# Kernel tuning notes

Measured on AMD Instinct MI355X. Metric: run time of the kernel, lower is better.

The kernel has to match this reference:

```python
import jax, jax.numpy as jnp
import numpy as np

N_NODES = 100000
N_EDGES = 3200000
IN_CH = 35
NUM_FAM = 26
EMBED = 8
NEW_IN = 6 + EMBED + (IN_CH - 6 - NUM_FAM)  # 17
HID = 64
LN_EPS = 1e-5


def setup_inputs() -> dict:
    key = jax.random.key(0)
    ks = jax.random.split(key, 16)
    x = jax.random.normal(ks[0], (N_NODES, IN_CH), dtype=jnp.float32)
    edge_index = jax.random.randint(ks[1], (2, N_EDGES), 0, N_NODES, dtype=jnp.int64)
    s = 0.05
    p = {
        'W_embed': jax.random.normal(ks[2], (NUM_FAM, EMBED), jnp.float32) * s,
        'b_embed': jnp.zeros((EMBED,), jnp.float32),
        'ln_g': jnp.ones((EMBED,), jnp.float32),
        'ln_b': jnp.zeros((EMBED,), jnp.float32),
        'Wl1': jax.random.normal(ks[3], (NEW_IN, HID), jnp.float32) * s,
        'bl1': jnp.zeros((HID,), jnp.float32),
        'Wr1': jax.random.normal(ks[4], (NEW_IN, HID), jnp.float32) * s,
        'Wl2': jax.random.normal(ks[5], (HID, HID), jnp.float32) * s,
        'bl2': jnp.zeros((HID,), jnp.float32),
        'Wr2': jax.random.normal(ks[6], (HID, HID), jnp.float32) * s,
        'Wl3': jax.random.normal(ks[7], (HID, HID), jnp.float32) * s,
        'bl3': jnp.zeros((HID,), jnp.float32),
        'Wr3': jax.random.normal(ks[8], (HID, HID), jnp.float32) * s,
        'Wfc': jax.random.normal(ks[9], (HID, 1), jnp.float32) * s,
        'bfc': jnp.zeros((1,), jnp.float32),
    }
    return {'x': x, 'edge_index': edge_index, **p}


def _sage(h, src, dst, Wl, bl, Wr, n):
    # PyG SAGEConv (mean aggr): lin_l(mean_{j in N(i)} h_j) + lin_r(h_i)
    msum = jax.ops.segment_sum(h[src], dst, num_segments=n)
    cnt = jax.ops.segment_sum(jnp.ones((src.shape[0],), h.dtype), dst, num_segments=n)
    mean = msum / jnp.maximum(cnt, 1.0)[:, None]
    return mean @ Wl + bl + h @ Wr


def reference(x, edge_index, W_embed, b_embed, ln_g, ln_b,
              Wl1, bl1, Wr1, Wl2, bl2, Wr2, Wl3, bl3, Wr3, Wfc, bfc):
    n = x.shape[0]
    src, dst = edge_index[0], edge_index[1]
    node_type = x[:, :6]
    onehot = x[:, 6:6 + NUM_FAM]
    other = x[:, 6 + NUM_FAM:]
    emb = onehot @ W_embed + b_embed
    mu = jnp.mean(emb, axis=-1, keepdims=True)
    var = jnp.var(emb, axis=-1, keepdims=True)
    emb = (emb - mu) * jax.lax.rsqrt(var + LN_EPS) * ln_g + ln_b
    h0 = jnp.concatenate([node_type, emb, other], axis=1)  # [N, 17]
    h1 = jax.nn.relu(_sage(h0, src, dst, Wl1, bl1, Wr1, n))
    h2 = jax.nn.relu(_sage(h1, src, dst, Wl2, bl2, Wr2, n) + h1)
    h3 = jax.nn.relu(_sage(h2, src, dst, Wl3, bl3, Wr3, n) + h2)
    return (h3 @ Wfc + bfc).squeeze(-1)
```

## Files before the change

kernel.cpp:

```cpp
#include <hip/hip_runtime.h>

#define NN 100000
#define NE 3200000
#define NBK 391
#define BCAP2 9216
#define EPB 4096
#define NPB 782

typedef _Float16 half8 __attribute__((ext_vector_type(8)));
typedef float    f32x4 __attribute__((ext_vector_type(4)));

__global__ __launch_bounds__(256) void k_h0(const float* __restrict__ x,
    const float* __restrict__ We, const float* __restrict__ be,
    const float* __restrict__ lg, const float* __restrict__ lb,
    _Float16* __restrict__ h0p)
{
  __shared__ float xs[256 * 35];
  int tid = threadIdx.x;
  int base_node = blockIdx.x * 256;
  int nvalid = NN - base_node; if (nvalid > 256) nvalid = 256;
  int total = nvalid * 35;
  const float* srcp = x + (size_t)base_node * 35;
  for (int j = tid; j < total; j += 256) xs[j] = srcp[j];
  __syncthreads();
  int i = base_node + tid;
  if (i >= NN) return;
  const float* xr = xs + tid * 35;
  float e[8];
  #pragma unroll
  for (int j = 0; j < 8; ++j) e[j] = be[j];
  #pragma unroll
  for (int k = 0; k < 26; ++k) {
    float o = xr[6 + k];
    #pragma unroll
    for (int j = 0; j < 8; ++j) e[j] = fmaf(o, We[k * 8 + j], e[j]);
  }
  float mu = 0.f;
  #pragma unroll
  for (int j = 0; j < 8; ++j) mu += e[j];
  mu *= 0.125f;
  float var = 0.f;
  #pragma unroll
  for (int j = 0; j < 8; ++j) { float d = e[j] - mu; var = fmaf(d, d, var); }
  var *= 0.125f;
  float rs = rsqrtf(var + 1e-5f);

  _Float16 row[32];
  #pragma unroll
  for (int j = 0; j < 6; ++j) row[j] = (_Float16)xr[j];
  #pragma unroll
  for (int j = 0; j < 8; ++j) row[6 + j] = (_Float16)((e[j] - mu) * rs * lg[j] + lb[j]);
  #pragma unroll
  for (int j = 0; j < 3; ++j) row[14 + j] = (_Float16)xr[32 + j];
  #pragma unroll
  for (int j = 17; j < 32; ++j) row[j] = (_Float16)0.f;
  half8* dst = (half8*)(h0p + (size_t)i * 32);
  #pragma unroll
  for (int q = 0; q < 4; ++q) dst[q] = *(half8*)(row + q * 8);
}

__global__ __launch_bounds__(256) void k_partA(const int* __restrict__ ei,
    int* __restrict__ gcur, int* __restrict__ ebuf)
{
  __shared__ int hist[NBK];
  __shared__ int lofs[NBK];
  __shared__ int gb[NBK];
  __shared__ int cur[NBK];
  __shared__ int sd[256];
  __shared__ int stage[EPB];
  __shared__ unsigned short sbkt[EPB];
  int tid = threadIdx.x;
  int base = blockIdx.x * EPB;
  int n = NE - base; if (n > EPB) n = EPB;
  for (int b = tid; b < NBK; b += 256) hist[b] = 0;
  __syncthreads();
  int s[16], d[16];
  #pragma unroll
  for (int k = 0; k < 16; ++k) {
    int idx = tid + k * 256;
    if (idx < n) {
      s[k] = ei[base + idx];
      d[k] = ei[NE + base + idx];
      atomicAdd(&hist[d[k] >> 8], 1);
    } else { s[k] = -1; d[k] = 0; }
  }
  __syncthreads();
  int b0 = 2 * tid, b1 = 2 * tid + 1;
  int c0 = (b0 < NBK) ? hist[b0] : 0;
  int c1 = (b1 < NBK) ? hist[b1] : 0;
  int ls = c0 + c1;
  sd[tid] = ls; __syncthreads();
  for (int off = 1; off < 256; off <<= 1) {
    int t = (tid >= off) ? sd[tid - off] : 0;
    __syncthreads(); sd[tid] += t; __syncthreads();
  }
  int excl = sd[tid] - ls;
  if (b0 < NBK) { lofs[b0] = excl;      cur[b0] = excl;      if (c0) gb[b0] = b0 * BCAP2 + atomicAdd(&gcur[b0], c0); }
  if (b1 < NBK) { lofs[b1] = excl + c0; cur[b1] = excl + c0; if (c1) gb[b1] = b1 * BCAP2 + atomicAdd(&gcur[b1], c1); }
  __syncthreads();
  #pragma unroll
  for (int k = 0; k < 16; ++k) {
    if (s[k] >= 0) {
      int b = d[k] >> 8;
      int p = atomicAdd(&cur[b], 1);
      stage[p] = (s[k] << 8) | (d[k] & 255);
      sbkt[p] = (unsigned short)b;
    }
  }
  __syncthreads();
  for (int p = tid; p < n; p += 256) {
    int b = sbkt[p];
    int pos = gb[b] + (p - lofs[b]);
    if (pos < (b + 1) * BCAP2) ebuf[pos] = stage[p];
  }
}

__global__ __launch_bounds__(512) void k_partB(const int* __restrict__ gcur,
    const int* __restrict__ ebuf, int2* __restrict__ rowinfo, int* __restrict__ srcs)
{
  __shared__ int lcnt[256];
  __shared__ int sd[256];
  int b = blockIdx.x, tid = threadIdx.x;
  int n = gcur[b]; if (n > BCAP2) n = BCAP2;
  const int* eb = ebuf + (size_t)b * BCAP2;
  if (tid < 256) lcnt[tid] = 0;
  __syncthreads();
  for (int e = tid; e < n; e += 512) atomicAdd(&lcnt[eb[e] & 255], 1);
  __syncthreads();
  int v = 0;
  if (tid < 256) { v = lcnt[tid]; sd[tid] = v; }
  __syncthreads();
  for (int off = 1; off < 256; off <<= 1) {
    int t = (tid < 256 && tid >= off) ? sd[tid - off] : 0;
    __syncthreads();
    if (tid < 256) sd[tid] += t;
    __syncthreads();
  }
  if (tid < 256) {
    int excl = sd[tid] - v;
    int node = b * 256 + tid;
    if (node < NN) rowinfo[node] = make_int2(b * BCAP2 + excl, v);
    lcnt[tid] = excl;
  }
  __syncthreads();
  for (int e = tid; e < n; e += 512) {
    int w = eb[e];
    int p = atomicAdd(&lcnt[w & 255], 1);
    srcs[(size_t)b * BCAP2 + p] = w >> 8;
  }
}

template <int W>
__global__ __launch_bounds__(256) void k_agg(const _Float16* __restrict__ hin,
    const int2* __restrict__ rowinfo, const int* __restrict__ srcs,
    _Float16* __restrict__ meanout)
{
  constexpr int GL = W / 8;
  constexpr int NPW = 64 / GL;
  int wave = (blockIdx.x * 256 + threadIdx.x) >> 6;
  int lane = threadIdx.x & 63;
  if (wave * NPW >= NN) return;
  int g = lane / GL;
  int f = lane % GL;
  int node = wave * NPW + g;
  bool valid = node < NN;
  int2 ri = valid ? rowinfo[node] : make_int2(0, 0);
  int rs = ri.x, m = ri.y;
  const int* __restrict__ sp = srcs + rs;

  float acc[8];
  #pragma unroll
  for (int q = 0; q < 8; ++q) acc[q] = 0.f;

  #pragma unroll 4
  for (int e = 0; e < m; ++e) {
    half8 v = *(const half8*)(hin + (size_t)sp[e] * W + f * 8);
    #pragma unroll
    for (int q = 0; q < 8; ++q) acc[q] += (float)v[q];
  }

  if (valid) {
    float r = 1.f / fmaxf((float)m, 1.f);
    _Float16 o[8];
    #pragma unroll
    for (int q = 0; q < 8; ++q) o[q] = (_Float16)(acc[q] * r);
    *(half8*)(meanout + (size_t)node * W + f * 8) = *(half8*)o;
  }
}

template <int W, int KW, bool RES, bool FINAL>
__global__ __launch_bounds__(256) void k_mlp(const _Float16* __restrict__ mean,
    const _Float16* __restrict__ h,
    const float* __restrict__ Wl, const float* __restrict__ bl,
    const float* __restrict__ Wr,
    const float* __restrict__ Wfc, const float* __restrict__ bfc,
    void* __restrict__ outp)
{
  __shared__ _Float16 lwl[64 * W];
  __shared__ _Float16 lwr[64 * W];
  int tid = threadIdx.x;
  for (int idx = tid; idx < 64 * W; idx += 256) {
    int nn = idx / W, kk = idx % W;
    lwl[idx] = (kk < KW) ? (_Float16)Wl[kk * 64 + nn] : (_Float16)0.f;
    lwr[idx] = (kk < KW) ? (_Float16)Wr[kk * 64 + nn] : (_Float16)0.f;
  }
  __syncthreads();
  constexpr int NKB = W / 32;
  int wv = tid >> 6, lane = tid & 63;
  int c = lane & 15, kg = lane >> 4;

  half8 bwl[4][NKB], bwr[4][NKB];
  #pragma unroll
  for (int nt = 0; nt < 4; ++nt)
    #pragma unroll
    for (int kb = 0; kb < NKB; ++kb) {
      bwl[nt][kb] = *(const half8*)&lwl[(nt * 16 + c) * W + kb * 32 + kg * 8];
      bwr[nt][kb] = *(const half8*)&lwr[(nt * 16 + c) * W + kb * 32 + kg * 8];
    }

  int wavebase = blockIdx.x * 256 + wv * 64;
  #pragma unroll
  for (int ti = 0; ti < 4; ++ti) {
    int tbase = wavebase + ti * 16;
    if (tbase >= NN) break;
    half8 am[NKB], ah[NKB];
    #pragma unroll
    for (int kb = 0; kb < NKB; ++kb) {
      am[kb] = *(const half8*)(mean + (size_t)(tbase + c) * W + kb * 32 + kg * 8);
      ah[kb] = *(const half8*)(h    + (size_t)(tbase + c) * W + kb * 32 + kg * 8);
    }
    f32x4 acc[4] = {f32x4{0,0,0,0}, f32x4{0,0,0,0}, f32x4{0,0,0,0}, f32x4{0,0,0,0}};
    #pragma unroll
    for (int nt = 0; nt < 4; ++nt)
      #pragma unroll
      for (int kb = 0; kb < NKB; ++kb) {
        acc[nt] = __builtin_amdgcn_mfma_f32_16x16x32_f16(am[kb], bwl[nt][kb], acc[nt], 0, 0, 0);
        acc[nt] = __builtin_amdgcn_mfma_f32_16x16x32_f16(ah[kb], bwr[nt][kb], acc[nt], 0, 0, 0);
      }
    if (!FINAL) {
      _Float16* hout = (_Float16*)outp;
      #pragma unroll
      for (int nt = 0; nt < 4; ++nt) {
        float bia = bl[nt * 16 + c];
        #pragma unroll
        for (int r = 0; r < 4; ++r) {
          int node = tbase + kg * 4 + r;
          float v = acc[nt][r] + bia;
          if (RES) v += (float)h[(size_t)node * 64 + nt * 16 + c];
          hout[(size_t)node * 64 + nt * 16 + c] = (_Float16)fmaxf(v, 0.f);
        }
      }
    } else {
      #pragma unroll
      for (int r = 0; r < 4; ++r) {
        float p = 0.f;
        #pragma unroll
        for (int nt = 0; nt < 4; ++nt) {
          float v = acc[nt][r] + bl[nt * 16 + c];
          if (RES) v += (float)h[(size_t)(tbase + kg * 4 + r) * 64 + nt * 16 + c];
          v = fmaxf(v, 0.f);
          p = fmaf(v, Wfc[nt * 16 + c], p);
        }
        p += __shfl_xor(p, 1); p += __shfl_xor(p, 2);
        p += __shfl_xor(p, 4); p += __shfl_xor(p, 8);
        if (c == 0) ((float*)outp)[tbase + kg * 4 + r] = p + bfc[0];
      }
    }
  }
}

extern "C" void kernel_launch(void* const* d_in, const int* in_sizes, int n_in,
                              void* d_out, int out_size, void* d_ws, size_t ws_size,
                              hipStream_t stream)
{
  const float* x   = (const float*)d_in[0];
  const int*   ei  = (const int*)d_in[1];
  const float* We  = (const float*)d_in[2];
  const float* be  = (const float*)d_in[3];
  const float* lg  = (const float*)d_in[4];
  const float* lb  = (const float*)d_in[5];
  const float* Wl1 = (const float*)d_in[6];
  const float* bl1 = (const float*)d_in[7];
  const float* Wr1 = (const float*)d_in[8];
  const float* Wl2 = (const float*)d_in[9];
  const float* bl2 = (const float*)d_in[10];
  const float* Wr2 = (const float*)d_in[11];
  const float* Wl3 = (const float*)d_in[12];
  const float* bl3 = (const float*)d_in[13];
  const float* Wr3 = (const float*)d_in[14];
  const float* Wfc = (const float*)d_in[15];
  const float* bfc = (const float*)d_in[16];
  (void)in_sizes; (void)n_in; (void)out_size; (void)ws_size;

  size_t off = 0;
  auto carve = [&](size_t bytes) -> void* {
    void* p = (char*)d_ws + off;
    off += (bytes + 255) & ~(size_t)255;
    return p;
  };
  _Float16* h0p    = (_Float16*)carve((size_t)NN * 32 * 2);
  _Float16* mean1  = (_Float16*)carve((size_t)NN * 32 * 2);
  char*     uni    = (char*)carve((size_t)NBK * BCAP2 * 4);
  int*      ebuf   = (int*)uni;
  _Float16* h1     = (_Float16*)uni;
  _Float16* mean23 = (_Float16*)carve((size_t)NN * 64 * 2);
  _Float16* h2     = (_Float16*)carve((size_t)NN * 64 * 2);
  int*      srcs   = (int*)carve((size_t)NBK * BCAP2 * 4);
  int2*     rowinfo= (int2*)carve((size_t)NN * 8);
  int*      gcur   = (int*)carve((size_t)NBK * 4);

  const int nblk_node  = (NN + 255) / 256;
  const int nblk_agg64 = ((NN + 7) / 8 + 3) / 4;
  const int nblk_agg32 = ((NN + 15) / 16 + 3) / 4;

  hipMemsetAsync(gcur, 0, (size_t)NBK * 4, stream);
  k_h0<<<nblk_node, 256, 0, stream>>>(x, We, be, lg, lb, h0p);
  k_partA<<<NPB, 256, 0, stream>>>(ei, gcur, ebuf);
  k_partB<<<NBK, 512, 0, stream>>>(gcur, ebuf, rowinfo, srcs);

  k_agg<32><<<nblk_agg32, 256, 0, stream>>>(h0p, rowinfo, srcs, mean1);
  k_mlp<32, 17, false, false><<<nblk_node, 256, 0, stream>>>(mean1, h0p, Wl1, bl1, Wr1, nullptr, nullptr, h1);
  k_agg<64><<<nblk_agg64, 256, 0, stream>>>(h1, rowinfo, srcs, mean23);
  k_mlp<64, 64, true, false><<<nblk_node, 256, 0, stream>>>(mean23, h1, Wl2, bl2, Wr2, nullptr, nullptr, h2);
  k_agg<64><<<nblk_agg64, 256, 0, stream>>>(h2, rowinfo, srcs, mean23);
  k_mlp<64, 64, true, true><<<nblk_node, 256, 0, stream>>>(mean23, h2, Wl3, bl3, Wr3, Wfc, bfc, d_out);
}
```

Before: 371.6 us.

## Sort nodes by degree within buckets and batch gather loads in aggregation

During CSR construction each bucket counting-sorts its nodes by in-degree into a permutation array. The aggregation kernels walk nodes through that permutation, so nodes sharing a wave have similar edge counts and lanes diverge less. The edge loop now loads eight neighbour indices and eight feature vectors before accumulating, giving more memory-level parallelism, and it uses shift-based addressing. In exchange it adds a serial prefix scan per block, an extra indirection per node, and output writes that are scattered rather than coalesced.

```diff
diff --git a/kernel.cpp b/kernel.cpp
--- a/kernel.cpp
+++ b/kernel.cpp
@@ -6,6 +6,7 @@
 #define BCAP2 9216
 #define EPB 4096
 #define NPB 782
+#define NSLOT (NBK * 256)
 
 typedef _Float16 half8 __attribute__((ext_vector_type(8)));
 typedef float    f32x4 __attribute__((ext_vector_type(4)));
@@ -116,18 +117,23 @@
 }
 
 __global__ __launch_bounds__(512) void k_partB(const int* __restrict__ gcur,
-    const int* __restrict__ ebuf, int2* __restrict__ rowinfo, int* __restrict__ srcs)
+    const int* __restrict__ ebuf, int2* __restrict__ rowinfo, int* __restrict__ srcs,
+    int* __restrict__ perm)
 {
   __shared__ int lcnt[256];
   __shared__ int sd[256];
+  __shared__ int dhist[128];
+  __shared__ int dcur[128];
   int b = blockIdx.x, tid = threadIdx.x;
   int n = gcur[b]; if (n > BCAP2) n = BCAP2;
   const int* eb = ebuf + (size_t)b * BCAP2;
   if (tid < 256) lcnt[tid] = 0;
+  if (tid >= 256 && tid < 384) dhist[tid - 256] = 0;
+  if (tid < 256) perm[b * 256 + tid] = -1;
   __syncthreads();
   for (int e = tid; e < n; e += 512) atomicAdd(&lcnt[eb[e] & 255], 1);
   __syncthreads();
-  int v = 0;
+  int v = 0, node = b * 256 + tid, dcl = 0;
   if (tid < 256) { v = lcnt[tid]; sd[tid] = v; }
   __syncthreads();
   for (int off = 1; off < 256; off <<= 1) {
@@ -138,11 +144,23 @@
   }
   if (tid < 256) {
     int excl = sd[tid] - v;
-    int node = b * 256 + tid;
-    if (node < NN) rowinfo[node] = make_int2(b * BCAP2 + excl, v);
+    if (node < NN) {
+      rowinfo[node] = make_int2(b * BCAP2 + excl, v);
+      dcl = v < 127 ? v : 127;
+      atomicAdd(&dhist[dcl], 1);
+    }
     lcnt[tid] = excl;
   }
   __syncthreads();
+  if (tid == 0) {
+    int run = 0;
+    for (int d = 0; d < 128; ++d) { int c = dhist[d]; dcur[d] = run; run += c; }
+  }
+  __syncthreads();
+  if (tid < 256 && node < NN) {
+    int p = atomicAdd(&dcur[dcl], 1);
+    perm[b * 256 + p] = node;
+  }
   for (int e = tid; e < n; e += 512) {
     int w = eb[e];
     int p = atomicAdd(&lcnt[w & 255], 1);
@@ -153,17 +171,18 @@
 template <int W>
 __global__ __launch_bounds__(256) void k_agg(const _Float16* __restrict__ hin,
     const int2* __restrict__ rowinfo, const int* __restrict__ srcs,
-    _Float16* __restrict__ meanout)
+    const int* __restrict__ perm, _Float16* __restrict__ meanout)
 {
   constexpr int GL = W / 8;
   constexpr int NPW = 64 / GL;
+  constexpr int SH = (W == 64) ? 6 : 5;
   int wave = (blockIdx.x * 256 + threadIdx.x) >> 6;
   int lane = threadIdx.x & 63;
-  if (wave * NPW >= NN) return;
-  int g = lane / GL;
+  int slot = wave * NPW + lane / GL;
+  if (wave * NPW >= NSLOT) return;
   int f = lane % GL;
-  int node = wave * NPW + g;
-  bool valid = node < NN;
+  int node = (slot < NSLOT) ? perm[slot] : -1;
+  bool valid = node >= 0;
   int2 ri = valid ? rowinfo[node] : make_int2(0, 0);
   int rs = ri.x, m = ri.y;
   const int* __restrict__ sp = srcs + rs;
@@ -172,9 +191,21 @@
   #pragma unroll
   for (int q = 0; q < 8; ++q) acc[q] = 0.f;
 
-  #pragma unroll 4
-  for (int e = 0; e < m; ++e) {
-    half8 v = *(const half8*)(hin + (size_t)sp[e] * W + f * 8);
+  int e = 0;
+  for (; e + 8 <= m; e += 8) {
+    int idx[8];
+    #pragma unroll
+    for (int t = 0; t < 8; ++t) idx[t] = sp[e + t];
+    half8 v[8];
+    #pragma unroll
+    for (int t = 0; t < 8; ++t) v[t] = *(const half8*)(hin + (idx[t] << SH) + f * 8);
+    #pragma unroll
+    for (int t = 0; t < 8; ++t)
+      #pragma unroll
+      for (int q = 0; q < 8; ++q) acc[q] += (float)v[t][q];
+  }
+  for (; e < m; ++e) {
+    half8 v = *(const half8*)(hin + (sp[e] << SH) + f * 8);
     #pragma unroll
     for (int q = 0; q < 8; ++q) acc[q] += (float)v[q];
   }
@@ -184,7 +215,7 @@
     _Float16 o[8];
     #pragma unroll
     for (int q = 0; q < 8; ++q) o[q] = (_Float16)(acc[q] * r);
-    *(half8*)(meanout + (size_t)node * W + f * 8) = *(half8*)o;
+    *(half8*)(meanout + ((size_t)node << SH) + f * 8) = *(half8*)o;
   }
 }
 
@@ -307,21 +338,22 @@
   _Float16* h2     = (_Float16*)carve((size_t)NN * 64 * 2);
   int*      srcs   = (int*)carve((size_t)NBK * BCAP2 * 4);
   int2*     rowinfo= (int2*)carve((size_t)NN * 8);
+  int*      perm   = (int*)carve((size_t)NSLOT * 4);
   int*      gcur   = (int*)carve((size_t)NBK * 4);
 
   const int nblk_node  = (NN + 255) / 256;
-  const int nblk_agg64 = ((NN + 7) / 8 + 3) / 4;
-  const int nblk_agg32 = ((NN + 15) / 16 + 3) / 4;
+  const int nblk_agg64 = (NSLOT / 8 + 3) / 4;
+  const int nblk_agg32 = (NSLOT / 16 + 3) / 4;
 
   hipMemsetAsync(gcur, 0, (size_t)NBK * 4, stream);
   k_h0<<<nblk_node, 256, 0, stream>>>(x, We, be, lg, lb, h0p);
   k_partA<<<NPB, 256, 0, stream>>>(ei, gcur, ebuf);
-  k_partB<<<NBK, 512, 0, stream>>>(gcur, ebuf, rowinfo, srcs);
-
-  k_agg<32><<<nblk_agg32, 256, 0, stream>>>(h0p, rowinfo, srcs, mean1);
+  k_partB<<<NBK, 512, 0, stream>>>(gcur, ebuf, rowinfo, srcs, perm);
+
+  k_agg<32><<<nblk_agg32, 256, 0, stream>>>(h0p, rowinfo, srcs, perm, mean1);
   k_mlp<32, 17, false, false><<<nblk_node, 256, 0, stream>>>(mean1, h0p, Wl1, bl1, Wr1, nullptr, nullptr, h1);
-  k_agg<64><<<nblk_agg64, 256, 0, stream>>>(h1, rowinfo, srcs, mean23);
+  k_agg<64><<<nblk_agg64, 256, 0, stream>>>(h1, rowinfo, srcs, perm, mean23);
   k_mlp<64, 64, true, false><<<nblk_node, 256, 0, stream>>>(mean23, h1, Wl2, bl2, Wr2, nullptr, nullptr, h2);
-  k_agg<64><<<nblk_agg64, 256, 0, stream>>>(h2, rowinfo, srcs, mean23);
+  k_agg<64><<<nblk_agg64, 256, 0, stream>>>(h2, rowinfo, srcs, perm, mean23);
   k_mlp<64, 64, true, true><<<nblk_node, 256, 0, stream>>>(mean23, h2, Wl3, bl3, Wr3, Wfc, bfc, d_out);
 }
```

New measurement: 391.1 us. 1.05x slower.
